# Kernel tuning notes

Hardware: AMD Instinct MI355X
Metric: run time of the kernel (lower is better)

The kernel has to match this reference:

```python
import jax, jax.numpy as jnp
import numpy as np

N = 100000      # nodes
E = 1600000     # edges
F_IN = 512      # input features
H = 64          # hidden
R = 2           # relations
B = 30          # bases
NEG_SLOPE = 0.2 # GATConv default


def setup_inputs() -> dict:
    key = jax.random.key(0)
    ks = jax.random.split(key, 14)
    s_in = 1.0 / np.sqrt(F_IN)
    s_h = 1.0 / np.sqrt(H)
    return {
        "x": jax.random.normal(ks[0], (N, F_IN), jnp.float32),
        "edge_index": jax.random.randint(ks[1], (2, E), 0, N),
        "edge_types": jax.random.randint(ks[2], (E,), 0, R),
        # RGCN layer 1 (F_IN -> H), basis-decomposed
        "basis1": jax.random.normal(ks[3], (B, F_IN, H), jnp.float32) * s_in,
        "comp1": jax.random.normal(ks[4], (R, B), jnp.float32) * (1.0 / np.sqrt(B)),
        "root1": jax.random.normal(ks[5], (F_IN, H), jnp.float32) * s_in,
        "bias1": jnp.zeros((H,), jnp.float32),
        # RGCN layer 2 (H -> H)
        "basis2": jax.random.normal(ks[6], (B, H, H), jnp.float32) * s_h,
        "comp2": jax.random.normal(ks[7], (R, B), jnp.float32) * (1.0 / np.sqrt(B)),
        "root2": jax.random.normal(ks[8], (H, H), jnp.float32) * s_h,
        "bias2": jnp.zeros((H,), jnp.float32),
        # GAT (H -> 1, heads=1)
        "gat_w": jax.random.normal(ks[9], (H, 1), jnp.float32) * s_h,
        "att_src": jax.random.normal(ks[10], (1,), jnp.float32),
        "att_dst": jax.random.normal(ks[11], (1,), jnp.float32),
        "gat_bias": jnp.zeros((1,), jnp.float32),
    }


def rgcn_layer(x, src, dst, etype, basis, comp, root, bias):
    # W_r = sum_b comp[r,b] * basis[b]; transform nodes once per relation,
    # then gather per edge (math-equal to PyG's per-edge transform, cheaper).
    W = jnp.einsum('rb,bio->rio', comp, basis)       # [R, in, out]
    h = jnp.einsum('ni,rio->rno', x, W)              # [R, N, out]
    out = x @ root + bias                            # root/self term
    for r in range(R):                               # R=2, fixed small loop
        m = (etype == r).astype(x.dtype)             # [E]
        msg = h[r][src] * m[:, None]                 # gather + mask
        agg = jax.ops.segment_sum(msg, dst, num_segments=N)
        cnt = jax.ops.segment_sum(m, dst, num_segments=N)
        out = out + agg / jnp.maximum(cnt, 1.0)[:, None]   # mean aggr per relation
    return out


def gat_layer(x, src, dst, gat_w, att_src, att_dst, gat_bias):
    # GATConv with heads=1, out=1, add_self_loops=True, negative_slope=0.2
    loop = jnp.arange(N)
    s = jnp.concatenate([src, loop])
    d = jnp.concatenate([dst, loop])
    h = x @ gat_w                                    # [N, 1]
    a_s = h[:, 0] * att_src[0]                       # [N]
    a_d = h[:, 0] * att_dst[0]                       # [N]
    e = jax.nn.leaky_relu(a_s[s] + a_d[d], NEG_SLOPE)  # [E+N]
    emax = jax.ops.segment_max(e, d, num_segments=N)   # every dst has self-loop
    ex = jnp.exp(e - emax[d])
    denom = jax.ops.segment_sum(ex, d, num_segments=N)
    alpha = ex / denom[d]                            # segment softmax over dst
    out = jax.ops.segment_sum(alpha[:, None] * h[s], d, num_segments=N)
    return out + gat_bias


def reference(x, edge_index, edge_types,
              basis1, comp1, root1, bias1,
              basis2, comp2, root2, bias2,
              gat_w, att_src, att_dst, gat_bias):
    src, dst = edge_index[0], edge_index[1]
    x1 = jax.nn.relu(rgcn_layer(x, src, dst, edge_types, basis1, comp1, root1, bias1))
    x2 = rgcn_layer(x1, src, dst, edge_types, basis2, comp2, root2, bias2)
    return gat_layer(x2, src, dst, gat_w, att_src, att_dst, gat_bias)  # [N, 1]
```

## Files before the change

### kernel.cpp

```cpp
#include <hip/hip_runtime.h>
#include <hip/hip_bf16.h>
#include <math.h>

#define NCOL 192
#define BB   30
#define SCAN_T 256
#define SCAN_ELEMS 1024

typedef short bf16x8 __attribute__((ext_vector_type(8)));
typedef float f32x4  __attribute__((ext_vector_type(4)));
typedef unsigned short u16x8 __attribute__((ext_vector_type(8)));

__device__ __forceinline__ ushort f2bf(float f) {
  unsigned u = __float_as_uint(f);
  unsigned r = u + 0x7fff + ((u >> 16) & 1);
  return (ushort)(r >> 16);
}
__device__ __forceinline__ float bf2f(ushort u) {
  return __uint_as_float(((unsigned)u) << 16);
}

__global__ void zero_int(int* __restrict__ p, int n) {
  int i = blockIdx.x * blockDim.x + threadIdx.x;
  if (i < n) p[i] = 0;
}

__global__ void hist_deg(const int* __restrict__ dst, int* __restrict__ deg, int E) {
  int e = blockIdx.x * blockDim.x + threadIdx.x;
  if (e >= E) return;
  atomicAdd(&deg[dst[e]], 1);
}

__global__ __launch_bounds__(SCAN_T) void scan_local(const int* __restrict__ deg,
                                                     int* __restrict__ rowptr,
                                                     int* __restrict__ partial, int N) {
  __shared__ int sdata[SCAN_T];
  int t = threadIdx.x;
  int base = blockIdx.x * SCAN_ELEMS + t * 4;
  int v[4], s = 0;
#pragma unroll
  for (int k = 0; k < 4; ++k) {
    v[k] = (base + k < N) ? deg[base + k] : 0;
    s += v[k];
  }
  sdata[t] = s;
  __syncthreads();
  for (int off = 1; off < SCAN_T; off <<= 1) {
    int add = (t >= off) ? sdata[t - off] : 0;
    __syncthreads();
    sdata[t] += add;
    __syncthreads();
  }
  int run = sdata[t] - s;
  if (t == SCAN_T - 1) partial[blockIdx.x] = sdata[t];
#pragma unroll
  for (int k = 0; k < 4; ++k) {
    if (base + k < N) rowptr[base + k] = run;
    run += v[k];
  }
}

__global__ __launch_bounds__(SCAN_T) void scan_partial(int* __restrict__ partial, int nb) {
  __shared__ int sdata[SCAN_T];
  int t = threadIdx.x;
  int v = (t < nb) ? partial[t] : 0;
  sdata[t] = v;
  __syncthreads();
  for (int off = 1; off < SCAN_T; off <<= 1) {
    int add = (t >= off) ? sdata[t - off] : 0;
    __syncthreads();
    sdata[t] += add;
    __syncthreads();
  }
  if (t < nb) partial[t] = sdata[t] - v;
  if (t == nb - 1) partial[nb] = sdata[t];
}

__global__ void scan_add(int* __restrict__ rowptr, const int* __restrict__ partial,
                         int* __restrict__ fill, int N) {
  int i = blockIdx.x * blockDim.x + threadIdx.x;
  if (i < N) {
    rowptr[i] += partial[i / SCAN_ELEMS];
    fill[i] = 0;
  }
  if (i == N) rowptr[N] = partial[(N + SCAN_ELEMS - 1) / SCAN_ELEMS];
}

__global__ void scatter_edges(const int* __restrict__ src, const int* __restrict__ dst,
                              const int* __restrict__ et, const int* __restrict__ rowptr,
                              int* __restrict__ fill, int* __restrict__ srcpk, int E) {
  int e = blockIdx.x * blockDim.x + threadIdx.x;
  if (e >= E) return;
  int d = dst[e];
  int pos = rowptr[d] + atomicAdd(&fill[d], 1);
  srcpk[pos] = src[e] | (et[e] << 30);
}

__global__ void build_wpk(const float* __restrict__ basis, const float* __restrict__ comp,
                          const float* __restrict__ root, ushort* __restrict__ Wpk, int Kin) {
  int idx = blockIdx.x * blockDim.x + threadIdx.x;
  if (idx >= Kin * NCOL) return;
  int k = idx / NCOL, j = idx - k * NCOL;
  float v;
  if (j < 64) {
    v = root[k * 64 + j];
  } else {
    int r = (j >> 6) - 1, o = j & 63;
    float s = 0.f;
#pragma unroll
    for (int b = 0; b < BB; ++b)
      s = fmaf(comp[r * BB + b], basis[((size_t)b * Kin + k) * 64 + o], s);
    v = s;
  }
  Wpk[(((size_t)(k >> 3) * NCOL + j) << 3) + (k & 7)] = f2bf(v);
}

template <int K, int BF16IN>
__global__ __launch_bounds__(256, 4) void gemm_mfma(const void* __restrict__ Xv,
                                                    const ushort* __restrict__ Wpk,
                                                    ushort* __restrict__ Y, int N) {
  constexpr int BK  = 64;
  constexpr int NC  = K / BK;
  constexpr int NLD = BF16IN ? (64 * (BK / 8) / 256) : (64 * (BK / 4) / 256);
  __shared__ ushort As[(NC > 1 ? 2 : 1) * 64 * BK];

  const int row0 = blockIdx.x * 64;
  const int tid  = threadIdx.x;
  const int wid  = tid >> 6;
  const int lane = tid & 63;
  const int lrow = lane & 15;
  const int lhi  = lane >> 4;

  const float*  Xf = (const float*)Xv;
  const ushort* Xh = (const ushort*)Xv;

  float4 pf[BF16IN ? 1 : NLD];
  u16x8  pfh[BF16IN ? NLD : 1];

#define LOAD_CHUNK(c)                                                              \
  if constexpr (BF16IN) {                                                          \
    _Pragma("unroll") for (int it = 0; it < NLD; ++it) {                           \
      int idx = tid + it * 256;                                                    \
      int row = idx / (BK / 8), kq = idx - row * (BK / 8);                         \
      int r = row0 + row;                                                          \
      pfh[it] = (u16x8){0, 0, 0, 0, 0, 0, 0, 0};                                   \
      if (r < N) pfh[it] = ((const u16x8*)Xh)[(size_t)r * (K / 8) + (c) * (BK / 8) + kq]; \
    }                                                                              \
  } else {                                                                         \
    _Pragma("unroll") for (int it = 0; it < NLD; ++it) {                           \
      int idx = tid + it * 256;                                                    \
      int row = idx / (BK / 4), kq = idx - row * (BK / 4);                         \
      int r = row0 + row;                                                          \
      pf[it] = make_float4(0.f, 0.f, 0.f, 0.f);                                    \
      if (r < N) pf[it] = ((const float4*)Xf)[(size_t)r * (K / 4) + (c) * (BK / 4) + kq]; \
    }                                                                              \
  }

#define COMMIT_CHUNK(buf)                                                          \
  {                                                                                \
    char* Aw = (char*)As + (size_t)(buf) * 64 * BK * 2;                            \
    if constexpr (BF16IN) {                                                        \
      _Pragma("unroll") for (int it = 0; it < NLD; ++it) {                         \
        int idx = tid + it * 256;                                                  \
        int row = idx / (BK / 8), kq = idx - row * (BK / 8);                       \
        int byte = ((row * BK + kq * 8) * 2) ^ ((row & 7) << 4);                   \
        *(u16x8*)(Aw + byte) = pfh[it];                                            \
      }                                                                            \
    } else {                                                                       \
      _Pragma("unroll") for (int it = 0; it < NLD; ++it) {                         \
        int idx = tid + it * 256;                                                  \
        int row = idx / (BK / 4), kq = idx - row * (BK / 4);                       \
        ushort4 b;                                                                 \
        b.x = f2bf(pf[it].x); b.y = f2bf(pf[it].y);                                \
        b.z = f2bf(pf[it].z); b.w = f2bf(pf[it].w);                                \
        int byte = ((row * BK + kq * 4) * 2) ^ ((row & 7) << 4);                   \
        *(ushort4*)(Aw + byte) = b;                                                \
      }                                                                            \
    }                                                                              \
  }

  LOAD_CHUNK(0)
  COMMIT_CHUNK(0)
  __syncthreads();

  f32x4 acc[4][3];
#pragma unroll
  for (int s = 0; s < 4; ++s)
#pragma unroll
    for (int c = 0; c < 3; ++c) acc[s][c] = (f32x4){0.f, 0.f, 0.f, 0.f};

  for (int c = 0; c < NC; ++c) {
    if (c + 1 < NC) { LOAD_CHUNK(c + 1) }
    const char* Ab = (const char*)As + (size_t)(NC > 1 ? (c & 1) : 0) * 64 * BK * 2;
#pragma unroll
    for (int t = 0; t < BK / 32; ++t) {
      int g = (c * (BK / 32) + t) * 4 + lhi;
      const bf16x8* bp = (const bf16x8*)Wpk + (size_t)g * NCOL + wid * 48 + lrow;
      bf16x8 b0 = bp[0];
      bf16x8 b1 = bp[16];
      bf16x8 b2 = bp[32];
      bf16x8 a[4];
#pragma unroll
      for (int s = 0; s < 4; ++s) {
        int arow = s * 16 + lrow;
        int abyte = ((arow * BK + t * 32 + lhi * 8) * 2) ^ ((arow & 7) << 4);
        a[s] = *(const bf16x8*)(Ab + abyte);
      }
#pragma unroll
      for (int s = 0; s < 4; ++s) {
        acc[s][0] = __builtin_amdgcn_mfma_f32_16x16x32_bf16(a[s], b0, acc[s][0], 0, 0, 0);
        acc[s][1] = __builtin_amdgcn_mfma_f32_16x16x32_bf16(a[s], b1, acc[s][1], 0, 0, 0);
        acc[s][2] = __builtin_amdgcn_mfma_f32_16x16x32_bf16(a[s], b2, acc[s][2], 0, 0, 0);
      }
    }
    if (c + 1 < NC) {
      __syncthreads();
      COMMIT_CHUNK((c + 1) & 1)
      __syncthreads();
    }
  }
#undef LOAD_CHUNK
#undef COMMIT_CHUNK

#pragma unroll
  for (int s = 0; s < 4; ++s) {
#pragma unroll
    for (int cc = 0; cc < 3; ++cc) {
#pragma unroll
      for (int j = 0; j < 4; ++j) {
        int r = row0 + s * 16 + lhi * 4 + j;
        if (r < N) Y[(size_t)r * NCOL + wid * 48 + cc * 16 + lrow] = f2bf(acc[s][cc][j]);
      }
    }
  }
}

template <int RELU, int GATH>
__global__ __launch_bounds__(256) void fused_agg(const ushort* __restrict__ Y,
                                                 const int* __restrict__ rowptr,
                                                 const int* __restrict__ srcpk,
                                                 const float* __restrict__ bias,
                                                 const float* __restrict__ gw,
                                                 ushort* __restrict__ accout,
                                                 float* __restrict__ hval, int N) {
  int n = blockIdx.x * 4 + (threadIdx.x >> 6);
  if (n >= N) return;
  const int lane = threadIdx.x & 63;
  const int g    = lane >> 3;
  const int f0   = (lane & 7) * 8;

  float a0[8], a1[8];
#pragma unroll
  for (int j = 0; j < 8; ++j) { a0[j] = 0.f; a1[j] = 0.f; }
  float c0 = 0.f, c1 = 0.f;

  const int beg = rowptr[n], end = rowptr[n + 1];
  for (int i = beg; i < end; i += 16) {
    int eA = i + g, eB = i + 8 + g;
    bool vA = eA < end, vB = eB < end;
    int pkA = 0, pkB = 0;
    if (vA) pkA = srcpk[eA];
    if (vB) pkB = srcpk[eB];
    u16x8 xA = (u16x8){0, 0, 0, 0, 0, 0, 0, 0}, xB = xA;
    if (vA) xA = *(const u16x8*)(Y + (size_t)(pkA & 0x3fffffff) * NCOL + 64 +
                                 ((pkA >> 30) << 6) + f0);
    if (vB) xB = *(const u16x8*)(Y + (size_t)(pkB & 0x3fffffff) * NCOL + 64 +
                                 ((pkB >> 30) << 6) + f0);
    float rA = (vA && (pkA >> 30)) ? 1.f : 0.f;
    float sA = vA ? 1.f : 0.f;
    float rB = (vB && (pkB >> 30)) ? 1.f : 0.f;
    float sB = vB ? 1.f : 0.f;
    c0 += (sA - rA) + (sB - rB);
    c1 += rA + rB;
#pragma unroll
    for (int j = 0; j < 8; ++j) {
      float fA = bf2f(xA[j]), fB = bf2f(xB[j]);
      a0[j] += (sA - rA) * fA + (sB - rB) * fB;
      a1[j] += rA * fA + rB * fB;
    }
  }

#pragma unroll
  for (int msk = 8; msk <= 32; msk <<= 1) {
#pragma unroll
    for (int j = 0; j < 8; ++j) {
      a0[j] += __shfl_xor(a0[j], msk);
      a1[j] += __shfl_xor(a1[j], msk);
    }
    c0 += __shfl_xor(c0, msk);
    c1 += __shfl_xor(c1, msk);
  }

  float inv0 = 1.f / fmaxf(c0, 1.f);
  float inv1 = 1.f / fmaxf(c1, 1.f);
  u16x8 rv = *(const u16x8*)(Y + (size_t)n * NCOL + f0);
  float4 bA = *(const float4*)(bias + f0);
  float4 bB = *(const float4*)(bias + f0 + 4);
  float bb[8] = {bA.x, bA.y, bA.z, bA.w, bB.x, bB.y, bB.z, bB.w};
  float res[8];
#pragma unroll
  for (int j = 0; j < 8; ++j) {
    float v = bf2f(rv[j]) + bb[j] + a0[j] * inv0 + a1[j] * inv1;
    res[j] = RELU ? fmaxf(v, 0.f) : v;
  }
  if (accout && g == 0) {
    u16x8 o;
#pragma unroll
    for (int j = 0; j < 8; ++j) o[j] = f2bf(res[j]);
    *(u16x8*)(accout + (size_t)n * 64 + f0) = o;
  }
  if (GATH) {
    float4 gA = *(const float4*)(gw + f0);
    float4 gB = *(const float4*)(gw + f0 + 4);
    float gg[8] = {gA.x, gA.y, gA.z, gA.w, gB.x, gB.y, gB.z, gB.w};
    float dot = 0.f;
#pragma unroll
    for (int j = 0; j < 8; ++j) dot = fmaf(res[j], gg[j], dot);
    dot += __shfl_xor(dot, 1);
    dot += __shfl_xor(dot, 2);
    dot += __shfl_xor(dot, 4);
    if (lane == 0) hval[n] = dot;
  }
}

__device__ __forceinline__ float leaky(float x) { return x > 0.f ? x : 0.2f * x; }

__global__ __launch_bounds__(256) void gat_csr(const int* __restrict__ rowptr,
                                               const int* __restrict__ srcpk,
                                               const float* __restrict__ hval,
                                               const float* __restrict__ as_,
                                               const float* __restrict__ ad_,
                                               const float* __restrict__ gb,
                                               float* __restrict__ out, int N) {
  int n = blockIdx.x * 4 + (threadIdx.x >> 6);
  if (n >= N) return;
  const int lane = threadIdx.x & 63;
  float as = *as_, ad = *ad_;
  float hv = hval[n];
  float adn = hv * ad;
  float eself = leaky(hv * as + adn);
  int beg = rowptr[n], end = rowptr[n + 1];
  int deg = end - beg;
  float m, den, acc;
  if (deg <= 64) {
    bool valid = lane < deg;
    float hs = 0.f;
    if (valid) hs = hval[srcpk[beg + lane] & 0x3fffffff];
    float e = valid ? leaky(hs * as + adn) : -3.4e38f;
    m = fmaxf(e, eself);
#pragma unroll
    for (int o = 32; o > 0; o >>= 1) m = fmaxf(m, __shfl_xor(m, o));
    float ex = valid ? expf(e - m) : 0.f;
    den = ex;
    acc = ex * hs;
#pragma unroll
    for (int o = 32; o > 0; o >>= 1) {
      den += __shfl_xor(den, o);
      acc += __shfl_xor(acc, o);
    }
  } else {
    m = eself;
    for (int i = beg + lane; i < end; i += 64)
      m = fmaxf(m, leaky(hval[srcpk[i] & 0x3fffffff] * as + adn));
#pragma unroll
    for (int o = 32; o > 0; o >>= 1) m = fmaxf(m, __shfl_xor(m, o));
    float dl = 0.f, al = 0.f;
    for (int i = beg + lane; i < end; i += 64) {
      float hs = hval[srcpk[i] & 0x3fffffff];
      float ex = expf(leaky(hs * as + adn) - m);
      dl += ex;
      al += ex * hs;
    }
    den = dl;
    acc = al;
#pragma unroll
    for (int o = 32; o > 0; o >>= 1) {
      den += __shfl_xor(den, o);
      acc += __shfl_xor(acc, o);
    }
  }
  float es = expf(eself - m);
  den += es;
  acc += es * hv;
  if (lane == 0) out[n] = acc / den + *gb;
}

extern "C" void kernel_launch(void* const* d_in, const int* in_sizes, int n_in,
                              void* d_out, int out_size, void* d_ws, size_t ws_size,
                              hipStream_t stream) {
  const float* x      = (const float*)d_in[0];
  const int*   eidx   = (const int*)d_in[1];
  const int*   etype  = (const int*)d_in[2];
  const float* basis1 = (const float*)d_in[3];
  const float* comp1  = (const float*)d_in[4];
  const float* root1  = (const float*)d_in[5];
  const float* bias1  = (const float*)d_in[6];
  const float* basis2 = (const float*)d_in[7];
  const float* comp2  = (const float*)d_in[8];
  const float* root2  = (const float*)d_in[9];
  const float* bias2  = (const float*)d_in[10];
  const float* gat_w  = (const float*)d_in[11];
  const float* att_s  = (const float*)d_in[12];
  const float* att_d  = (const float*)d_in[13];
  const float* gat_b  = (const float*)d_in[14];

  const int N = in_sizes[0] / 512;
  const int E = in_sizes[1] / 2;
  const int* src = eidx;
  const int* dst = eidx + E;

  char* p = (char*)d_ws;
  ushort* Y    = (ushort*)p; p += (size_t)N * NCOL * 2;
  ushort* acc1 = (ushort*)p; p += (size_t)N * 64 * 2;
  ushort* Wpk  = (ushort*)p; p += (size_t)512 * NCOL * 2;
  float* hval  = (float*)p;  p += (size_t)N * 4;
  int* deg     = (int*)p;    p += (size_t)N * 4;
  int* rowptr  = (int*)p;    p += (size_t)(N + 16) * 4;
  int* partial = (int*)p;    p += (size_t)(SCAN_T + 16) * 4;
  int* srcpk   = (int*)p;    p += (size_t)E * 4;
  float* out   = (float*)d_out;
  int* fill    = deg;

  const int TB = 256;
  const int GB = (N + 63) / 64;
  const int nb = (N + SCAN_ELEMS - 1) / SCAN_ELEMS;

  zero_int<<<(N + TB - 1) / TB, TB, 0, stream>>>(deg, N);
  hist_deg<<<(E + TB - 1) / TB, TB, 0, stream>>>(dst, deg, E);
  scan_local<<<nb, SCAN_T, 0, stream>>>(deg, rowptr, partial, N);
  scan_partial<<<1, SCAN_T, 0, stream>>>(partial, nb);
  scan_add<<<(N + 1 + TB - 1) / TB, TB, 0, stream>>>(rowptr, partial, fill, N);
  scatter_edges<<<(E + TB - 1) / TB, TB, 0, stream>>>(src, dst, etype, rowptr, fill, srcpk, E);

  build_wpk<<<(512 * NCOL + TB - 1) / TB, TB, 0, stream>>>(basis1, comp1, root1, Wpk, 512);
  gemm_mfma<512, 0><<<GB, 256, 0, stream>>>(x, Wpk, Y, N);
  fused_agg<1, 0><<<(N + 3) / 4, TB, 0, stream>>>(Y, rowptr, srcpk, bias1, nullptr, acc1,
                                                  nullptr, N);

  build_wpk<<<(64 * NCOL + TB - 1) / TB, TB, 0, stream>>>(basis2, comp2, root2, Wpk, 64);
  gemm_mfma<64, 1><<<GB, 256, 0, stream>>>(acc1, Wpk, Y, N);
  fused_agg<0, 1><<<(N + 3) / 4, TB, 0, stream>>>(Y, rowptr, srcpk, bias2, gat_w, nullptr,
                                                  hval, N);

  gat_csr<<<(N + 3) / 4, TB, 0, stream>>>(rowptr, srcpk, hval, att_s, att_d, gat_b,
                                          out, N);
}
```

Before: 410.7 us.

## Cut launches and deepen GEMM prefetch to two chunks in flight

Drops the scan_add pass by having consumers add the block partial offset to rowptr on the fly. Zeroes deg and fill with a single memset, and builds both layers' packed weights in one launch. The layer-1 GEMM now holds global loads two chunks ahead in alternating register sets, which removes one barrier per iteration. This trades fewer launches and less sync for extra registers and an extra partial lookup in every aggregation kernel.

```diff
diff --git a/kernel.cpp b/kernel.cpp
--- a/kernel.cpp
+++ b/kernel.cpp
@@ -18,11 +18,6 @@
 }
 __device__ __forceinline__ float bf2f(ushort u) {
   return __uint_as_float(((unsigned)u) << 16);
-}
-
-__global__ void zero_int(int* __restrict__ p, int n) {
-  int i = blockIdx.x * blockDim.x + threadIdx.x;
-  if (i < n) p[i] = 0;
 }
 
 __global__ void hist_deg(const int* __restrict__ dst, int* __restrict__ deg, int E) {
@@ -55,7 +50,7 @@
   if (t == SCAN_T - 1) partial[blockIdx.x] = sdata[t];
 #pragma unroll
   for (int k = 0; k < 4; ++k) {
-    if (base + k < N) rowptr[base + k] = run;
+    if (base + k <= N) rowptr[base + k] = run;
     run += v[k];
   }
 }
@@ -76,30 +71,21 @@
   if (t == nb - 1) partial[nb] = sdata[t];
 }
 
-__global__ void scan_add(int* __restrict__ rowptr, const int* __restrict__ partial,
-                         int* __restrict__ fill, int N) {
-  int i = blockIdx.x * blockDim.x + threadIdx.x;
-  if (i < N) {
-    rowptr[i] += partial[i / SCAN_ELEMS];
-    fill[i] = 0;
-  }
-  if (i == N) rowptr[N] = partial[(N + SCAN_ELEMS - 1) / SCAN_ELEMS];
-}
-
 __global__ void scatter_edges(const int* __restrict__ src, const int* __restrict__ dst,
                               const int* __restrict__ et, const int* __restrict__ rowptr,
+                              const int* __restrict__ partial,
                               int* __restrict__ fill, int* __restrict__ srcpk, int E) {
   int e = blockIdx.x * blockDim.x + threadIdx.x;
   if (e >= E) return;
   int d = dst[e];
-  int pos = rowptr[d] + atomicAdd(&fill[d], 1);
+  int pos = rowptr[d] + partial[d >> 10] + atomicAdd(&fill[d], 1);
   srcpk[pos] = src[e] | (et[e] << 30);
 }
 
-__global__ void build_wpk(const float* __restrict__ basis, const float* __restrict__ comp,
-                          const float* __restrict__ root, ushort* __restrict__ Wpk, int Kin) {
-  int idx = blockIdx.x * blockDim.x + threadIdx.x;
-  if (idx >= Kin * NCOL) return;
+__device__ __forceinline__ void wpk_one(const float* __restrict__ basis,
+                                        const float* __restrict__ comp,
+                                        const float* __restrict__ root,
+                                        ushort* __restrict__ Wpk, int Kin, int idx) {
   int k = idx / NCOL, j = idx - k * NCOL;
   float v;
   if (j < 64) {
@@ -113,6 +99,20 @@
     v = s;
   }
   Wpk[(((size_t)(k >> 3) * NCOL + j) << 3) + (k & 7)] = f2bf(v);
+}
+
+__global__ void build_wpk_both(const float* __restrict__ basis1, const float* __restrict__ comp1,
+                               const float* __restrict__ root1,
+                               const float* __restrict__ basis2, const float* __restrict__ comp2,
+                               const float* __restrict__ root2,
+                               ushort* __restrict__ Wpk1, ushort* __restrict__ Wpk2) {
+  int idx = blockIdx.x * blockDim.x + threadIdx.x;
+  if (idx < 512 * NCOL) {
+    wpk_one(basis1, comp1, root1, Wpk1, 512, idx);
+  } else {
+    idx -= 512 * NCOL;
+    if (idx < 64 * NCOL) wpk_one(basis2, comp2, root2, Wpk2, 64, idx);
+  }
 }
 
 template <int K, int BF16IN>
@@ -134,53 +134,54 @@
   const float*  Xf = (const float*)Xv;
   const ushort* Xh = (const ushort*)Xv;
 
-  float4 pf[BF16IN ? 1 : NLD];
-  u16x8  pfh[BF16IN ? NLD : 1];
-
-#define LOAD_CHUNK(c)                                                              \
-  if constexpr (BF16IN) {                                                          \
-    _Pragma("unroll") for (int it = 0; it < NLD; ++it) {                           \
-      int idx = tid + it * 256;                                                    \
-      int row = idx / (BK / 8), kq = idx - row * (BK / 8);                         \
-      int r = row0 + row;                                                          \
-      pfh[it] = (u16x8){0, 0, 0, 0, 0, 0, 0, 0};                                   \
-      if (r < N) pfh[it] = ((const u16x8*)Xh)[(size_t)r * (K / 8) + (c) * (BK / 8) + kq]; \
-    }                                                                              \
-  } else {                                                                         \
-    _Pragma("unroll") for (int it = 0; it < NLD; ++it) {                           \
-      int idx = tid + it * 256;                                                    \
-      int row = idx / (BK / 4), kq = idx - row * (BK / 4);                         \
-      int r = row0 + row;                                                          \
-      pf[it] = make_float4(0.f, 0.f, 0.f, 0.f);                                    \
-      if (r < N) pf[it] = ((const float4*)Xf)[(size_t)r * (K / 4) + (c) * (BK / 4) + kq]; \
-    }                                                                              \
-  }
-
-#define COMMIT_CHUNK(buf)                                                          \
-  {                                                                                \
-    char* Aw = (char*)As + (size_t)(buf) * 64 * BK * 2;                            \
-    if constexpr (BF16IN) {                                                        \
-      _Pragma("unroll") for (int it = 0; it < NLD; ++it) {                         \
-        int idx = tid + it * 256;                                                  \
-        int row = idx / (BK / 8), kq = idx - row * (BK / 8);                       \
-        int byte = ((row * BK + kq * 8) * 2) ^ ((row & 7) << 4);                   \
-        *(u16x8*)(Aw + byte) = pfh[it];                                            \
-      }                                                                            \
-    } else {                                                                       \
-      _Pragma("unroll") for (int it = 0; it < NLD; ++it) {                         \
-        int idx = tid + it * 256;                                                  \
-        int row = idx / (BK / 4), kq = idx - row * (BK / 4);                       \
-        ushort4 b;                                                                 \
-        b.x = f2bf(pf[it].x); b.y = f2bf(pf[it].y);                                \
-        b.z = f2bf(pf[it].z); b.w = f2bf(pf[it].w);                                \
-        int byte = ((row * BK + kq * 4) * 2) ^ ((row & 7) << 4);                   \
-        *(ushort4*)(Aw + byte) = b;                                                \
-      }                                                                            \
-    }                                                                              \
-  }
-
-  LOAD_CHUNK(0)
-  COMMIT_CHUNK(0)
+  float4 pfA[BF16IN ? 1 : NLD], pfB[BF16IN ? 1 : NLD];
+  u16x8  phA[BF16IN ? NLD : 1], phB[BF16IN ? NLD : 1];
+
+#define LOAD_CHUNK(c, PF, PH)                                                       \
+  if constexpr (BF16IN) {                                                           \
+    _Pragma("unroll") for (int it = 0; it < NLD; ++it) {                            \
+      int idx = tid + it * 256;                                                     \
+      int row = idx / (BK / 8), kq = idx - row * (BK / 8);                          \
+      int r = row0 + row;                                                           \
+      PH[it] = (u16x8){0, 0, 0, 0, 0, 0, 0, 0};                                     \
+      if (r < N) PH[it] = ((const u16x8*)Xh)[(size_t)r * (K / 8) + (c) * (BK / 8) + kq]; \
+    }                                                                               \
+  } else {                                                                          \
+    _Pragma("unroll") for (int it = 0; it < NLD; ++it) {                            \
+      int idx = tid + it * 256;                                                     \
+      int row = idx / (BK / 4), kq = idx - row * (BK / 4);                          \
+      int r = row0 + row;                                                           \
+      PF[it] = make_float4(0.f, 0.f, 0.f, 0.f);                                     \
+      if (r < N) PF[it] = ((const float4*)Xf)[(size_t)r * (K / 4) + (c) * (BK / 4) + kq]; \
+    }                                                                               \
+  }
+
+#define COMMIT_CHUNK(buf, PF, PH)                                                   \
+  {                                                                                 \
+    char* Aw = (char*)As + (size_t)(buf) * 64 * BK * 2;                             \
+    if constexpr (BF16IN) {                                                         \
+      _Pragma("unroll") for (int it = 0; it < NLD; ++it) {                          \
+        int idx = tid + it * 256;                                                   \
+        int row = idx / (BK / 8), kq = idx - row * (BK / 8);                        \
+        int byte = ((row * BK + kq * 8) * 2) ^ ((row & 7) << 4);                    \
+        *(u16x8*)(Aw + byte) = PH[it];                                              \
+      }                                                                             \
+    } else {                                                                        \
+      _Pragma("unroll") for (int it = 0; it < NLD; ++it) {                          \
+        int idx = tid + it * 256;                                                   \
+        int row = idx / (BK / 4), kq = idx - row * (BK / 4);                        \
+        ushort4 b;                                                                  \
+        b.x = f2bf(PF[it].x); b.y = f2bf(PF[it].y);                                 \
+        b.z = f2bf(PF[it].z); b.w = f2bf(PF[it].w);                                 \
+        int byte = ((row * BK + kq * 4) * 2) ^ ((row & 7) << 4);                    \
+        *(ushort4*)(Aw + byte) = b;                                                 \
+      }                                                                             \
+    }                                                                               \
+  }
+
+  LOAD_CHUNK(0, pfA, phA)
+  COMMIT_CHUNK(0, pfA, phA)
+  if constexpr (NC > 1) { LOAD_CHUNK(1, pfB, phB) }
   __syncthreads();
 
   f32x4 acc[4][3];
@@ -189,8 +190,12 @@
 #pragma unroll
     for (int c = 0; c < 3; ++c) acc[s][c] = (f32x4){0.f, 0.f, 0.f, 0.f};
 
+#pragma unroll
   for (int c = 0; c < NC; ++c) {
-    if (c + 1 < NC) { LOAD_CHUNK(c + 1) }
+    if (c + 2 < NC) {
+      if ((c & 1) == 0) { LOAD_CHUNK(c + 2, pfA, phA) }
+      else              { LOAD_CHUNK(c + 2, pfB, phB) }
+    }
     const char* Ab = (const char*)As + (size_t)(NC > 1 ? (c & 1) : 0) * 64 * BK * 2;
 #pragma unroll
     for (int t = 0; t < BK / 32; ++t) {
@@ -214,8 +219,8 @@
       }
     }
     if (c + 1 < NC) {
-      __syncthreads();
-      COMMIT_CHUNK((c + 1) & 1)
+      if (((c + 1) & 1) == 0) { COMMIT_CHUNK(0, pfA, phA) }
+      else                    { COMMIT_CHUNK(1, pfB, phB) }
       __syncthreads();
     }
   }
@@ -238,6 +243,7 @@
 template <int RELU, int GATH>
 __global__ __launch_bounds__(256) void fused_agg(const ushort* __restrict__ Y,
                                                  const int* __restrict__ rowptr,
+                                                 const int* __restrict__ partial,
                                                  const int* __restrict__ srcpk,
                                                  const float* __restrict__ bias,
                                                  const float* __restrict__ gw,
@@ -254,7 +260,8 @@
   for (int j = 0; j < 8; ++j) { a0[j] = 0.f; a1[j] = 0.f; }
   float c0 = 0.f, c1 = 0.f;
 
-  const int beg = rowptr[n], end = rowptr[n + 1];
+  const int beg = rowptr[n] + partial[n >> 10];
+  const int end = rowptr[n + 1] + partial[(n + 1) >> 10];
   for (int i = beg; i < end; i += 16) {
     int eA = i + g, eB = i + 8 + g;
     bool vA = eA < end, vB = eB < end;
@@ -326,6 +333,7 @@
 __device__ __forceinline__ float leaky(float x) { return x > 0.f ? x : 0.2f * x; }
 
 __global__ __launch_bounds__(256) void gat_csr(const int* __restrict__ rowptr,
+                                               const int* __restrict__ partial,
                                                const int* __restrict__ srcpk,
                                                const float* __restrict__ hval,
                                                const float* __restrict__ as_,
@@ -339,7 +347,8 @@
   float hv = hval[n];
   float adn = hv * ad;
   float eself = leaky(hv * as + adn);
-  int beg = rowptr[n], end = rowptr[n + 1];
+  const int beg = rowptr[n] + partial[n >> 10];
+  const int end = rowptr[n + 1] + partial[(n + 1) >> 10];
   int deg = end - beg;
   float m, den, acc;
   if (deg <= 64) {
@@ -412,36 +421,39 @@
   char* p = (char*)d_ws;
   ushort* Y    = (ushort*)p; p += (size_t)N * NCOL * 2;
   ushort* acc1 = (ushort*)p; p += (size_t)N * 64 * 2;
-  ushort* Wpk  = (ushort*)p; p += (size_t)512 * NCOL * 2;
+  ushort* Wpk1 = (ushort*)p; p += (size_t)512 * NCOL * 2;
+  ushort* Wpk2 = (ushort*)p; p += (size_t)64 * NCOL * 2;
   float* hval  = (float*)p;  p += (size_t)N * 4;
   int* deg     = (int*)p;    p += (size_t)N * 4;
+  int* fill    = (int*)p;    p += (size_t)N * 4;
   int* rowptr  = (int*)p;    p += (size_t)(N + 16) * 4;
   int* partial = (int*)p;    p += (size_t)(SCAN_T + 16) * 4;
   int* srcpk   = (int*)p;    p += (size_t)E * 4;
   float* out   = (float*)d_out;
-  int* fill    = deg;
 
   const int TB = 256;
   const int GB = (N + 63) / 64;
-  const int nb = (N + SCAN_ELEMS - 1) / SCAN_ELEMS;
-
-  zero_int<<<(N + TB - 1) / TB, TB, 0, stream>>>(deg, N);
+  const int nb = (N + 1 + SCAN_ELEMS - 1) / SCAN_ELEMS;
+
+  hipMemsetAsync(deg, 0, (size_t)2 * N * sizeof(int), stream);
   hist_deg<<<(E + TB - 1) / TB, TB, 0, stream>>>(dst, deg, E);
   scan_local<<<nb, SCAN_T, 0, stream>>>(deg, rowptr, partial, N);
   scan_partial<<<1, SCAN_T, 0, stream>>>(partial, nb);
-  scan_add<<<(N + 1 + TB - 1) / TB, TB, 0, stream>>>(rowptr, partial, fill, N);
-  scatter_edges<<<(E + TB - 1) / TB, TB, 0, stream>>>(src, dst, etype, rowptr, fill, srcpk, E);
-
-  build_wpk<<<(512 * NCOL + TB - 1) / TB, TB, 0, stream>>>(basis1, comp1, root1, Wpk, 512);
-  gemm_mfma<512, 0><<<GB, 256, 0, stream>>>(x, Wpk, Y, N);
-  fused_agg<1, 0><<<(N + 3) / 4, TB, 0, stream>>>(Y, rowptr, srcpk, bias1, nullptr, acc1,
-                                                  nullptr, N);
-
-  build_wpk<<<(64 * NCOL + TB - 1) / TB, TB, 0, stream>>>(basis2, comp2, root2, Wpk, 64);
-  gemm_mfma<64, 1><<<GB, 256, 0, stream>>>(acc1, Wpk, Y, N);
-  fused_agg<0, 1><<<(N + 3) / 4, TB, 0, stream>>>(Y, rowptr, srcpk, bias2, gat_w, nullptr,
-                                                  hval, N);
-
-  gat_csr<<<(N + 3) / 4, TB, 0, stream>>>(rowptr, srcpk, hval, att_s, att_d, gat_b,
+  scatter_edges<<<(E + TB - 1) / TB, TB, 0, stream>>>(src, dst, etype, rowptr, partial,
+                                                      fill, srcpk, E);
+
+  build_wpk_both<<<(576 * NCOL + TB - 1) / TB, TB, 0, stream>>>(basis1, comp1, root1,
+                                                                basis2, comp2, root2,
+                                                                Wpk1, Wpk2);
+
+  gemm_mfma<512, 0><<<GB, 256, 0, stream>>>(x, Wpk1, Y, N);
+  fused_agg<1, 0><<<(N + 3) / 4, TB, 0, stream>>>(Y, rowptr, partial, srcpk, bias1, nullptr,
+                                                  acc1, nullptr, N);
+
+  gemm_mfma<64, 1><<<GB, 256, 0, stream>>>(acc1, Wpk2, Y, N);
+  fused_agg<0, 1><<<(N + 3) / 4, TB, 0, stream>>>(Y, rowptr, partial, srcpk, bias2, gat_w,
+                                                  nullptr, hval, N);
+
+  gat_csr<<<(N + 3) / 4, TB, 0, stream>>>(rowptr, partial, srcpk, hval, att_s, att_d, gat_b,
                                           out, N);
 }
```

After: 420.7 us, median of 3. 2.4% more time.
